# Optimization experiments

Measured on AMD Instinct MI355X. Metric: run time of the kernel, lower is better.

## Reference

```python
import jax, jax.numpy as jnp
import numpy as np

N_NODES = 5
B, C, H, W = 4, 256, 32, 32
THRESH = 0.3
EPS = 1e-12


def setup_inputs() -> dict:
    key = jax.random.key(0)
    k1, k2, k3, k4 = jax.random.split(key, 4)
    x = jax.random.normal(k1, (N_NODES, B, C, H, W), dtype=jnp.float32)
    w = jax.random.normal(k2, (N_NODES, N_NODES), dtype=jnp.float32)
    # 5 stacked conv1x1 'experts': Conv2d(2C -> C, k=1) weight [C,2C] + bias [C]
    conv_w = jax.random.normal(k3, (N_NODES, C, 2 * C), dtype=jnp.float32) * 0.02
    conv_b = jax.random.normal(k4, (N_NODES, C), dtype=jnp.float32) * 0.02
    return {"x": x, "w": w, "conv_w": conv_w, "conv_b": conv_b}


def reference(x, w, conv_w, conv_b):
    # x: [N, B, C, H, W] -- the list of N node feature maps stacked
    N, b, c, h, ww = x.shape
    P = b * c * h * ww  # 'pixels' = total element count of one node tensor

    # conv_i(cat(node_j, node_i + node_j)) splits into W1@node_j + W2@(node_i+node_j) + b_i
    W1 = conv_w[:, :, :c]          # [N, C, C] acts on node_j
    W2 = conv_w[:, :, c:]          # [N, C, C] acts on node_i + node_j
    A = W1 + W2                    # combined weight on node_j

    term_j = jnp.einsum('ick,jbkhw->ijbchw', A, x)    # [N,N,B,C,H,W]
    term_i = jnp.einsum('ick,ibkhw->ibchw', W2, x)    # [N,B,C,H,W]
    target = term_j + term_i[:, None] + conv_b[:, None, None, :, None, None]
    distance = x[None, :] - target                    # distance[i,j] = node_j - conv_i(...)

    # edge_list[:, i, j] = flatten(distance[i, j])  -> [P, N, N]
    edge = distance.reshape(N, N, P).transpose(2, 0, 1)

    # new_edge = edge * w; sigmoid; threshold at 0.3; L2-normalize over dim=2 (j axis)
    e = jax.nn.sigmoid(edge * w)
    e = jnp.where(e > THRESH, e, jnp.zeros_like(e))
    norm = jnp.sqrt(jnp.sum(e * e, axis=2, keepdims=True))
    e = e / jnp.maximum(norm, EPS)

    # node matrix: [P, N] of flattened node features; fuse h[p,i] = sum_j e[p,i,j]*node[p,j]
    node = x.reshape(N, P).T
    hmat = jnp.einsum('pij,pj->pi', e, node)          # [P, N]
    return hmat.T.reshape(N, b, c, h, ww)
```

## Files before the change

### kernel.cpp

```cpp
#include <hip/hip_runtime.h>
#include <cmath>

#define NN  5
#define BB  4
#define CCH 256
#define HWD 1024
#define THRESH_V 0.3f
#define EPS_V 1e-12f

#define CT 32
#define WT 32
#define KC 32
#define APAD 36
#define SPAD 36

#define SMEM_FLOATS 7424

__global__ __launch_bounds__(384, 4)
void fub_main(const float* __restrict__ x, const float* __restrict__ wmat,
              const float* __restrict__ conv_w, const float* __restrict__ conv_b,
              float* __restrict__ out)
{
    __shared__ __align__(16) float smem[SMEM_FLOATS];
    float* Xs  = smem;
    float* As  = smem + 5120;
    float* W2s = smem + 6272;
    float* Es  = smem;

    const int tid  = threadIdx.x;
    const int wv   = tid >> 6;
    const int lane = tid & 63;

    int bid = blockIdx.x;
    const int hwt = bid & 31; bid >>= 5;
    const int b   = bid & 3;  bid >>= 2;
    const int ct  = bid & 7;  bid >>= 3;
    const int i   = bid;

    const int c0  = ct * CT;
    const int hw0 = hwt * WT;

    const int lr = (lane >> 3) << 2;
    const int lc = (lane & 7)  << 2;

    const int jx = (wv < 5) ? wv : i;
    const float* M = (wv == 5) ? W2s : As;
    const float* Mb = M + lr;
    const float* Xb = Xs + jx * (KC * WT) + lc;

    float acc[4][4];
#pragma unroll
    for (int r = 0; r < 4; ++r)
#pragma unroll
        for (int c = 0; c < 4; ++c) acc[r][c] = 0.0f;

    for (int k0 = 0; k0 < CCH; k0 += KC) {
        if (tid < 320) {
#pragma unroll
            for (int it = 0; it < 4; ++it) {
                const int t   = tid + it * 320;
                const int j   = t >> 8;
                const int rem = t & 255;
                const int kk  = rem >> 3;
                const int p4  = (rem & 7) << 2;
                const float4 v = *(const float4*)(
                    x + (size_t)((j * BB + b) * CCH + k0 + kk) * HWD + hw0 + p4);
                *(float4*)(Xs + j * (KC * WT) + kk * WT + p4) = v;
            }
        } else {
            const int u = tid - 320;
#pragma unroll
            for (int it = 0; it < 4; ++it) {
                const int t  = u + (it << 6);
                const int r  = t >> 3;
                const int kq = (t & 7) << 2;
                const float* base =
                    conv_w + (size_t)(i * CCH + c0 + r) * (2 * CCH) + k0 + kq;
                const float4 w1 = *(const float4*)(base);
                const float4 w2 = *(const float4*)(base + CCH);
                As [(kq + 0) * APAD + r] = w1.x + w2.x;
                As [(kq + 1) * APAD + r] = w1.y + w2.y;
                As [(kq + 2) * APAD + r] = w1.z + w2.z;
                As [(kq + 3) * APAD + r] = w1.w + w2.w;
                W2s[(kq + 0) * APAD + r] = w2.x;
                W2s[(kq + 1) * APAD + r] = w2.y;
                W2s[(kq + 2) * APAD + r] = w2.z;
                W2s[(kq + 3) * APAD + r] = w2.w;
            }
        }
        __syncthreads();

#pragma unroll
        for (int kk = 0; kk < KC; ++kk) {
            const float4 a  = *(const float4*)(Mb + kk * APAD);
            const float4 xv = *(const float4*)(Xb + kk * WT);
            const float ar[4] = {a.x, a.y, a.z, a.w};
            const float xc[4] = {xv.x, xv.y, xv.z, xv.w};
#pragma unroll
            for (int r = 0; r < 4; ++r)
#pragma unroll
                for (int c = 0; c < 4; ++c)
                    acc[r][c] = fmaf(ar[r], xc[c], acc[r][c]);
        }
        __syncthreads();
    }

#pragma unroll
    for (int r = 0; r < 4; ++r) {
        *(float4*)(Es + wv * (CT * SPAD) + (lr + r) * SPAD + lc) =
            make_float4(acc[r][0], acc[r][1], acc[r][2], acc[r][3]);
    }
    __syncthreads();

    if (tid < 256) {
        const int row = tid >> 3;
        const int col = (tid & 7) << 2;
        const int c   = c0 + row;
        const float bias = conv_b[i * CCH + c];

        float wrow[NN];
#pragma unroll
        for (int j = 0; j < NN; ++j) wrow[j] = wmat[i * NN + j];

        const float4 T = *(const float4*)(Es + 5 * (CT * SPAD) + row * SPAD + col);
        const float Tv[4] = {T.x, T.y, T.z, T.w};

        float num[4] = {0.f, 0.f, 0.f, 0.f};
        float sq [4] = {0.f, 0.f, 0.f, 0.f};
#pragma unroll
        for (int j = 0; j < NN; ++j) {
            const float4 s  = *(const float4*)(Es + j * (CT * SPAD) + row * SPAD + col);
            const float4 xj = *(const float4*)(
                x + (size_t)((j * BB + b) * CCH + c) * HWD + hw0 + col);
            const float sv[4] = {s.x, s.y, s.z, s.w};
            const float xv[4] = {xj.x, xj.y, xj.z, xj.w};
#pragma unroll
            for (int cc = 0; cc < 4; ++cc) {
                const float target = sv[cc] + Tv[cc] + bias;
                const float dist   = xv[cc] - target;
                const float z      = dist * wrow[j];
                float e = 1.0f / (1.0f + expf(-z));
                e = (e > THRESH_V) ? e : 0.0f;
                sq[cc]  = fmaf(e, e, sq[cc]);
                num[cc] = fmaf(e, xv[cc], num[cc]);
            }
        }
        float res[4];
#pragma unroll
        for (int cc = 0; cc < 4; ++cc)
            res[cc] = num[cc] / fmaxf(sqrtf(sq[cc]), EPS_V);

        *(float4*)(out + (size_t)((i * BB + b) * CCH + c) * HWD + hw0 + col) =
            make_float4(res[0], res[1], res[2], res[3]);
    }
}

extern "C" void kernel_launch(void* const* d_in, const int* in_sizes, int n_in,
                              void* d_out, int out_size, void* d_ws, size_t ws_size,
                              hipStream_t stream) {
    const float* x      = (const float*)d_in[0];
    const float* w      = (const float*)d_in[1];
    const float* conv_w = (const float*)d_in[2];
    const float* conv_b = (const float*)d_in[3];
    float* out = (float*)d_out;

    dim3 grid(5120);
    dim3 block(384);
    fub_main<<<grid, block, 0, stream>>>(x, w, conv_w, conv_b, out);
}
```

Before: 360.6 us.

## Enlarge GEMM tile to 64x64 with 8x8 per-thread register blocking

Doubles the channel and pixel tile sizes so each thread computes an 8x8 accumulator block instead of 4x4, raising arithmetic intensity per shared-memory load and cutting the grid to a quarter of the blocks. The weight loader is restructured to write transposed float4s, and the epilogue is split into two 32-row halves so the staging buffer fits. This costs more registers and shared memory per block, and occupancy drops to fewer resident blocks.

```diff
diff --git a/kernel.cpp b/kernel.cpp
--- a/kernel.cpp
+++ b/kernel.cpp
@@ -8,23 +8,26 @@
 #define THRESH_V 0.3f
 #define EPS_V 1e-12f
 
-#define CT 32
-#define WT 32
+#define CT 64
+#define WT 64
 #define KC 32
-#define APAD 36
-#define SPAD 36
+#define APAD 68
+#define SPAD 68
 
-#define SMEM_FLOATS 7424
+#define XS_FLOATS (NN * KC * WT)
+#define AS_OFF    XS_FLOATS
+#define W2_OFF    (AS_OFF + KC * APAD)
+#define SMEM_FLOATS (W2_OFF + KC * APAD)
 
-__global__ __launch_bounds__(384, 4)
+__global__ __launch_bounds__(384, 3)
 void fub_main(const float* __restrict__ x, const float* __restrict__ wmat,
               const float* __restrict__ conv_w, const float* __restrict__ conv_b,
               float* __restrict__ out)
 {
     __shared__ __align__(16) float smem[SMEM_FLOATS];
     float* Xs  = smem;
-    float* As  = smem + 5120;
-    float* W2s = smem + 6272;
+    float* As  = smem + AS_OFF;
+    float* W2s = smem + W2_OFF;
     float* Es  = smem;
 
     const int tid  = threadIdx.x;
@@ -32,126 +35,149 @@
     const int lane = tid & 63;
 
     int bid = blockIdx.x;
-    const int hwt = bid & 31; bid >>= 5;
+    const int hwt = bid & 15; bid >>= 4;
     const int b   = bid & 3;  bid >>= 2;
-    const int ct  = bid & 7;  bid >>= 3;
+    const int ct  = bid & 3;  bid >>= 2;
     const int i   = bid;
 
     const int c0  = ct * CT;
     const int hw0 = hwt * WT;
 
-    const int lr = (lane >> 3) << 2;
-    const int lc = (lane & 7)  << 2;
+    const int lr = (lane >> 3) << 3;
+    const int lc = (lane & 7)  << 3;
 
     const int jx = (wv < 5) ? wv : i;
-    const float* M = (wv == 5) ? W2s : As;
+    const float* M  = (wv == 5) ? W2s : As;
     const float* Mb = M + lr;
     const float* Xb = Xs + jx * (KC * WT) + lc;
 
-    float acc[4][4];
+    float acc[8][8];
 #pragma unroll
-    for (int r = 0; r < 4; ++r)
+    for (int r = 0; r < 8; ++r)
 #pragma unroll
-        for (int c = 0; c < 4; ++c) acc[r][c] = 0.0f;
+        for (int c = 0; c < 8; ++c) acc[r][c] = 0.0f;
 
     for (int k0 = 0; k0 < CCH; k0 += KC) {
-        if (tid < 320) {
+        if (tid < 256) {
 #pragma unroll
-            for (int it = 0; it < 4; ++it) {
-                const int t   = tid + it * 320;
-                const int j   = t >> 8;
-                const int rem = t & 255;
-                const int kk  = rem >> 3;
-                const int p4  = (rem & 7) << 2;
+            for (int it = 0; it < 10; ++it) {
+                const int t   = tid + it * 256;
+                const int j   = t >> 9;
+                const int rem = t & 511;
+                const int kk  = rem >> 4;
+                const int q4  = (rem & 15) << 2;
                 const float4 v = *(const float4*)(
-                    x + (size_t)((j * BB + b) * CCH + k0 + kk) * HWD + hw0 + p4);
-                *(float4*)(Xs + j * (KC * WT) + kk * WT + p4) = v;
+                    x + (size_t)((j * BB + b) * CCH + k0 + kk) * HWD + hw0 + q4);
+                *(float4*)(Xs + j * (KC * WT) + kk * WT + q4) = v;
             }
         } else {
-            const int u = tid - 320;
+            const int u   = tid - 256;
+            const int rq  = u >> 3;
+            const int kq4 = (u & 7) << 2;
+            const int rb  = rq << 2;
+            const float* base0 =
+                conv_w + (size_t)(i * CCH + c0 + rb) * (2 * CCH) + k0 + kq4;
+            float4 w1[4], w2[4];
 #pragma unroll
-            for (int it = 0; it < 4; ++it) {
-                const int t  = u + (it << 6);
-                const int r  = t >> 3;
-                const int kq = (t & 7) << 2;
-                const float* base =
-                    conv_w + (size_t)(i * CCH + c0 + r) * (2 * CCH) + k0 + kq;
-                const float4 w1 = *(const float4*)(base);
-                const float4 w2 = *(const float4*)(base + CCH);
-                As [(kq + 0) * APAD + r] = w1.x + w2.x;
-                As [(kq + 1) * APAD + r] = w1.y + w2.y;
-                As [(kq + 2) * APAD + r] = w1.z + w2.z;
-                As [(kq + 3) * APAD + r] = w1.w + w2.w;
-                W2s[(kq + 0) * APAD + r] = w2.x;
-                W2s[(kq + 1) * APAD + r] = w2.y;
-                W2s[(kq + 2) * APAD + r] = w2.z;
-                W2s[(kq + 3) * APAD + r] = w2.w;
+            for (int rr = 0; rr < 4; ++rr) {
+                w1[rr] = *(const float4*)(base0 + rr * (2 * CCH));
+                w2[rr] = *(const float4*)(base0 + rr * (2 * CCH) + CCH);
             }
+            *(float4*)(As + (kq4 + 0) * APAD + rb) = make_float4(
+                w1[0].x + w2[0].x, w1[1].x + w2[1].x, w1[2].x + w2[2].x, w1[3].x + w2[3].x);
+            *(float4*)(As + (kq4 + 1) * APAD + rb) = make_float4(
+                w1[0].y + w2[0].y, w1[1].y + w2[1].y, w1[2].y + w2[2].y, w1[3].y + w2[3].y);
+            *(float4*)(As + (kq4 + 2) * APAD + rb) = make_float4(
+                w1[0].z + w2[0].z, w1[1].z + w2[1].z, w1[2].z + w2[2].z, w1[3].z + w2[3].z);
+            *(float4*)(As + (kq4 + 3) * APAD + rb) = make_float4(
+                w1[0].w + w2[0].w, w1[1].w + w2[1].w, w1[2].w + w2[2].w, w1[3].w + w2[3].w);
+            *(float4*)(W2s + (kq4 + 0) * APAD + rb) = make_float4(w2[0].x, w2[1].x, w2[2].x, w2[3].x);
+            *(float4*)(W2s + (kq4 + 1) * APAD + rb) = make_float4(w2[0].y, w2[1].y, w2[2].y, w2[3].y);
+            *(float4*)(W2s + (kq4 + 2) * APAD + rb) = make_float4(w2[0].z, w2[1].z, w2[2].z, w2[3].z);
+            *(float4*)(W2s + (kq4 + 3) * APAD + rb) = make_float4(w2[0].w, w2[1].w, w2[2].w, w2[3].w);
         }
         __syncthreads();
 
+#pragma unroll 4
+        for (int kk = 0; kk < KC; ++kk) {
+            const float4 a0  = *(const float4*)(Mb + kk * APAD);
+            const float4 a1  = *(const float4*)(Mb + kk * APAD + 4);
+            const float4 xv0 = *(const float4*)(Xb + kk * WT);
+            const float4 xv1 = *(const float4*)(Xb + kk * WT + 4);
+            const float ar[8] = {a0.x, a0.y, a0.z, a0.w, a1.x, a1.y, a1.z, a1.w};
+            const float xc[8] = {xv0.x, xv0.y, xv0.z, xv0.w, xv1.x, xv1.y, xv1.z, xv1.w};
 #pragma unroll
-        for (int kk = 0; kk < KC; ++kk) {
-            const float4 a  = *(const float4*)(Mb + kk * APAD);
-            const float4 xv = *(const float4*)(Xb + kk * WT);
-            const float ar[4] = {a.x, a.y, a.z, a.w};
-            const float xc[4] = {xv.x, xv.y, xv.z, xv.w};
+            for (int r = 0; r < 8; ++r)
 #pragma unroll
-            for (int r = 0; r < 4; ++r)
-#pragma unroll
-                for (int c = 0; c < 4; ++c)
+                for (int c = 0; c < 8; ++c)
                     acc[r][c] = fmaf(ar[r], xc[c], acc[r][c]);
         }
         __syncthreads();
     }
 
+    const int rhme  = lr >> 5;
+    const int rbase = lr & 31;
+
 #pragma unroll
-    for (int r = 0; r < 4; ++r) {
-        *(float4*)(Es + wv * (CT * SPAD) + (lr + r) * SPAD + lc) =
-            make_float4(acc[r][0], acc[r][1], acc[r][2], acc[r][3]);
-    }
-    __syncthreads();
-
-    if (tid < 256) {
-        const int row = tid >> 3;
-        const int col = (tid & 7) << 2;
-        const int c   = c0 + row;
-        const float bias = conv_b[i * CCH + c];
-
-        float wrow[NN];
+    for (int rh = 0; rh < 2; ++rh) {
+        if (rhme == rh) {
+            float* Eb = Es + wv * (32 * SPAD) + lc;
 #pragma unroll
-        for (int j = 0; j < NN; ++j) wrow[j] = wmat[i * NN + j];
-
-        const float4 T = *(const float4*)(Es + 5 * (CT * SPAD) + row * SPAD + col);
-        const float Tv[4] = {T.x, T.y, T.z, T.w};
-
-        float num[4] = {0.f, 0.f, 0.f, 0.f};
-        float sq [4] = {0.f, 0.f, 0.f, 0.f};
-#pragma unroll
-        for (int j = 0; j < NN; ++j) {
-            const float4 s  = *(const float4*)(Es + j * (CT * SPAD) + row * SPAD + col);
-            const float4 xj = *(const float4*)(
-                x + (size_t)((j * BB + b) * CCH + c) * HWD + hw0 + col);
-            const float sv[4] = {s.x, s.y, s.z, s.w};
-            const float xv[4] = {xj.x, xj.y, xj.z, xj.w};
-#pragma unroll
-            for (int cc = 0; cc < 4; ++cc) {
-                const float target = sv[cc] + Tv[cc] + bias;
-                const float dist   = xv[cc] - target;
-                const float z      = dist * wrow[j];
-                float e = 1.0f / (1.0f + expf(-z));
-                e = (e > THRESH_V) ? e : 0.0f;
-                sq[cc]  = fmaf(e, e, sq[cc]);
-                num[cc] = fmaf(e, xv[cc], num[cc]);
+            for (int r = 0; r < 8; ++r) {
+                *(float4*)(Eb + (rbase + r) * SPAD) =
+                    make_float4(acc[r][0], acc[r][1], acc[r][2], acc[r][3]);
+                *(float4*)(Eb + (rbase + r) * SPAD + 4) =
+                    make_float4(acc[r][4], acc[r][5], acc[r][6], acc[r][7]);
             }
         }
-        float res[4];
+        __syncthreads();
+
+        if (tid < 256) {
+            const int row = tid >> 3;
+            const int c   = c0 + rh * 32 + row;
+            const float bias = conv_b[i * CCH + c];
+
+            float wrow[NN];
 #pragma unroll
-        for (int cc = 0; cc < 4; ++cc)
-            res[cc] = num[cc] / fmaxf(sqrtf(sq[cc]), EPS_V);
+            for (int j = 0; j < NN; ++j) wrow[j] = wmat[i * NN + j];
 
-        *(float4*)(out + (size_t)((i * BB + b) * CCH + c) * HWD + hw0 + col) =
-            make_float4(res[0], res[1], res[2], res[3]);
+            const int colA = (tid & 7) << 2;
+#pragma unroll
+            for (int half = 0; half < 2; ++half) {
+                const int col = colA + (half << 5);
+
+                const float4 T = *(const float4*)(Es + 5 * (32 * SPAD) + row * SPAD + col);
+                const float Tv[4] = {T.x, T.y, T.z, T.w};
+
+                float num[4] = {0.f, 0.f, 0.f, 0.f};
+                float sq [4] = {0.f, 0.f, 0.f, 0.f};
+#pragma unroll
+                for (int j = 0; j < NN; ++j) {
+                    const float4 s  = *(const float4*)(Es + j * (32 * SPAD) + row * SPAD + col);
+                    const float4 xj = *(const float4*)(
+                        x + (size_t)((j * BB + b) * CCH + c) * HWD + hw0 + col);
+                    const float sv[4] = {s.x, s.y, s.z, s.w};
+                    const float xv[4] = {xj.x, xj.y, xj.z, xj.w};
+#pragma unroll
+                    for (int cc = 0; cc < 4; ++cc) {
+                        const float target = sv[cc] + Tv[cc] + bias;
+                        const float dist   = xv[cc] - target;
+                        const float z      = dist * wrow[j];
+                        float e = 1.0f / (1.0f + expf(-z));
+                        e = (e > THRESH_V) ? e : 0.0f;
+                        sq[cc]  = fmaf(e, e, sq[cc]);
+                        num[cc] = fmaf(e, xv[cc], num[cc]);
+                    }
+                }
+                float4 res;
+                res.x = num[0] / fmaxf(sqrtf(sq[0]), EPS_V);
+                res.y = num[1] / fmaxf(sqrtf(sq[1]), EPS_V);
+                res.z = num[2] / fmaxf(sqrtf(sq[2]), EPS_V);
+                res.w = num[3] / fmaxf(sqrtf(sq[3]), EPS_V);
+                *(float4*)(out + (size_t)((i * BB + b) * CCH + c) * HWD + hw0 + col) = res;
+            }
+        }
+        __syncthreads();
     }
 }
 
@@ -164,7 +190,7 @@
     const float* conv_b = (const float*)d_in[3];
     float* out = (float*)d_out;
 
-    dim3 grid(5120);
+    dim3 grid(1280);
     dim3 block(384);
     fub_main<<<grid, block, 0, stream>>>(x, w, conv_w, conv_b, out);
 }
```

Result: faster. 330.6 us (-8.3%).
